# Performance work log

Measured on AMD Instinct MI355X. Metric: run time of the kernel, lower is better.

## Reference

```python
import jax, jax.numpy as jnp
import numpy as np

N, E = 50000, 800000
IN_F, HID, NCLS, NLAYERS = 64, 64, 2, 3
BN_EPS = 1e-5


def batch_norm(x, gamma, beta):
    # training-mode BatchNorm1d: biased batch statistics over the node/edge dim
    m = jnp.mean(x, axis=0)
    v = jnp.var(x, axis=0)
    return gamma * (x - m) * jax.lax.rsqrt(v + BN_EPS) + beta


def setup_inputs() -> dict:
    key = jax.random.key(0)
    ks = jax.random.split(key, 24)
    L, Lp1 = NLAYERS, NLAYERS + 1

    def lin(k, fan_in, shape):
        bound = 1.0 / np.sqrt(fan_in)
        return jax.random.uniform(k, shape, jnp.float32, -bound, bound)

    return {
        "h": jax.random.normal(ks[0], (N, IN_F), jnp.float32),
        "src": jax.random.randint(ks[1], (E,), 0, N, jnp.int32),
        "dst": jax.random.randint(ks[2], (E,), 0, N, jnp.int32),
        "emb_W": lin(ks[3], IN_F, (IN_F, HID)),
        "emb_b": lin(ks[4], IN_F, (HID,)),
        "mlp_W1": lin(ks[5], HID, (L, HID, HID)),
        "mlp_b1": lin(ks[6], HID, (L, HID)),
        "mlp_bn_g": jnp.ones((L, HID), jnp.float32),
        "mlp_bn_b": jnp.zeros((L, HID), jnp.float32),
        "mlp_W2": lin(ks[7], HID, (L, HID, HID)),
        "mlp_b2": lin(ks[8], HID, (L, HID)),
        "apply_bn_g": jnp.ones((L, HID), jnp.float32),
        "apply_bn_b": jnp.zeros((L, HID), jnp.float32),
        "out_bn_g": jnp.ones((L, HID), jnp.float32),
        "out_bn_b": jnp.zeros((L, HID), jnp.float32),
        "pred_W1": lin(ks[9], 2 * HID, (Lp1, 2 * HID, HID)),
        "pred_b1": lin(ks[10], 2 * HID, (Lp1, HID)),
        "pred_W2": lin(ks[11], HID, (Lp1, HID, NCLS)),
        "pred_b2": lin(ks[12], HID, (Lp1, NCLS)),
    }


def reference(h, src, dst, emb_W, emb_b, mlp_W1, mlp_b1, mlp_bn_g, mlp_bn_b,
              mlp_W2, mlp_b2, apply_bn_g, apply_bn_b, out_bn_g, out_bn_b,
              pred_W1, pred_b1, pred_W2, pred_b2):
    n_layers = mlp_W1.shape[0]
    n_nodes = h.shape[0]

    def edge_feat(hn):
        # concat src and dst node features per edge -> [E, 2*HID]
        return jnp.concatenate([hn[src], hn[dst]], axis=1)

    hn = h @ emb_W + emb_b  # embedding_h
    edge_reps = [edge_feat(hn)]

    for i in range(n_layers):
        # GINConv (sum aggregation, eps=0): (1+eps)*h_v + sum_{u->v} h_u
        agg = jax.ops.segment_sum(hn[src], dst, num_segments=n_nodes)
        z = hn + agg
        # MLP (depth 2): Linear -> BN -> ReLU -> Linear
        z = jax.nn.relu(batch_norm(z @ mlp_W1[i] + mlp_b1[i], mlp_bn_g[i], mlp_bn_b[i]))
        z = z @ mlp_W2[i] + mlp_b2[i]
        # ApplyNodeFunc: BN + ReLU
        z = jax.nn.relu(batch_norm(z, apply_bn_g[i], apply_bn_b[i]))
        # outer per-layer BN + ReLU
        hn = jax.nn.relu(batch_norm(z, out_bn_g[i], out_bn_b[i]))
        edge_reps.append(edge_feat(hn))

    # sum of per-layer edge predictions: Linear(2h->h) -> ReLU -> Linear(h->ncls)
    score = jnp.zeros((src.shape[0], pred_W2.shape[-1]), h.dtype)
    for i, e in enumerate(edge_reps):
        score = score + jax.nn.relu(e @ pred_W1[i] + pred_b1[i]) @ pred_W2[i] + pred_b2[i]
    return score
```

## Files before the change

kernel.cpp:

```cpp
#include <hip/hip_runtime.h>
#include <hip/hip_bf16.h>


#define BN_EPS 1e-5f

static __device__ __forceinline__ float bf2f_lo(unsigned u) {
  return __uint_as_float(u << 16);
}
static __device__ __forceinline__ float bf2f_hi(unsigned u) {
  return __uint_as_float(u & 0xffff0000u);
}

__global__ __launch_bounds__(256) void hist_kernel(const int* __restrict__ dst,
                                                   int* __restrict__ deg, int E) {
  int i = blockIdx.x * blockDim.x + threadIdx.x;
  int stride = gridDim.x * blockDim.x;
  for (; i < E; i += stride) atomicAdd(&deg[dst[i]], 1);
}

__global__ __launch_bounds__(256) void scan1_kernel(const int* __restrict__ deg,
                                                    int* __restrict__ rowstart,
                                                    int* __restrict__ partials, int N) {
  __shared__ int wsum[4];
  int tid = threadIdx.x;
  int lane = tid & 63, w = tid >> 6;
  int base = blockIdx.x * 1024 + tid * 4;
  int d0 = 0, d1 = 0, d2 = 0, d3 = 0;
  if (base + 3 < N) {
    int4 v = *reinterpret_cast<const int4*>(deg + base);
    d0 = v.x; d1 = v.y; d2 = v.z; d3 = v.w;
  } else {
    if (base + 0 < N) d0 = deg[base + 0];
    if (base + 1 < N) d1 = deg[base + 1];
    if (base + 2 < N) d2 = deg[base + 2];
  }
  int t0 = d0, t1 = t0 + d1, t2 = t1 + d2, t3 = t2 + d3;
  int tot = t3;
  int inc = tot;
#pragma unroll
  for (int off = 1; off < 64; off <<= 1) {
    int v = __shfl_up(inc, off);
    if (lane >= off) inc += v;
  }
  if (lane == 63) wsum[w] = inc;
  __syncthreads();
  int woff = 0;
  for (int k = 0; k < w; ++k) woff += wsum[k];
  int excl = woff + inc - tot;
  if (base + 0 < N) rowstart[base + 0] = excl;
  if (base + 1 < N) rowstart[base + 1] = excl + t0;
  if (base + 2 < N) rowstart[base + 2] = excl + t1;
  if (base + 3 < N) rowstart[base + 3] = excl + t2;
  if (tid == 255) partials[blockIdx.x] = excl + t3;
}

__global__ __launch_bounds__(256) void scan3_kernel(const int* __restrict__ partials,
                                                    int* __restrict__ rowstart,
                                                    int* __restrict__ cursor,
                                                    int N, int NB, int E) {
  __shared__ int s_off;
  int tid = threadIdx.x;
  if (tid < 64) {
    int v = (tid < NB) ? partials[tid] : 0;
    int inc = v;
#pragma unroll
    for (int off = 1; off < 64; off <<= 1) {
      int t = __shfl_up(inc, off);
      if (tid >= off) inc += t;
    }
    if (tid == (int)blockIdx.x) s_off = inc - v;
  }
  __syncthreads();
  int off = s_off;
  int base = blockIdx.x * 1024 + tid * 4;
#pragma unroll
  for (int k = 0; k < 4; ++k) {
    int i = base + k;
    if (i < N) {
      int r = rowstart[i] + off;
      rowstart[i] = r;
      cursor[i] = r;
    }
  }
  if (blockIdx.x == 0 && tid == 0) rowstart[N] = E;
}

__global__ __launch_bounds__(256) void fill_kernel(const int* __restrict__ src,
                                                   const int* __restrict__ dst,
                                                   int* __restrict__ cursor,
                                                   int2* __restrict__ epack, int E) {
  int i = blockIdx.x * blockDim.x + threadIdx.x;
  int stride = gridDim.x * blockDim.x;
  for (; i < E; i += stride) {
    int p = atomicAdd(&cursor[dst[i]], 1);
    epack[p] = make_int2(src[i], i);
  }
}

__global__ __launch_bounds__(256) void gemm64_kernel(
    const float* __restrict__ in, const float* __restrict__ W,
    const float* __restrict__ bias, const float* __restrict__ stats_in,
    const float* __restrict__ g_in, const float* __restrict__ b_in,
    float* __restrict__ out, float* __restrict__ stats_out,
    ushort* __restrict__ out_g, int N) {
  __shared__ float sW[64][64];
  __shared__ float sx[32][64];
  __shared__ float red[2][4][64];
  int tid = threadIdx.x;
  int lane = tid & 63, w = tid >> 6;
  int n0 = blockIdx.x * 32;
#pragma unroll
  for (int r = 0; r < 16; ++r) {
    int idx = r * 256 + tid;
    sW[idx >> 6][idx & 63] = W[idx];
  }
  float sc = 1.f, sh = 0.f;
  if (stats_in) {
    float invN = 1.0f / (float)N;
    float m = stats_in[lane] * invN;
    float var = stats_in[64 + lane] * invN - m * m;
    sc = g_in[lane] * rsqrtf(var + BN_EPS);
    sh = b_in[lane] - m * sc;
  }
#pragma unroll
  for (int r = 0; r < 8; ++r) {
    int idx = r * 256 + tid;
    int n = n0 + (idx >> 6);
    float x = (n < N) ? in[(size_t)n * 64 + lane] : 0.f;
    if (stats_in) x = fmaxf(x * sc + sh, 0.f);
    sx[idx >> 6][lane] = x;
  }
  __syncthreads();
  float acc[8];
  float bz = bias ? bias[lane] : 0.f;
#pragma unroll
  for (int j = 0; j < 8; ++j) acc[j] = bz;
  for (int k = 0; k < 64; ++k) {
    float wv = sW[k][lane];
#pragma unroll
    for (int j = 0; j < 8; ++j) acc[j] = fmaf(sx[w * 8 + j][k], wv, acc[j]);
  }
  float ps = 0.f, pq = 0.f;
#pragma unroll
  for (int j = 0; j < 8; ++j) {
    int n = n0 + w * 8 + j;
    if (n < N) {
      out[(size_t)n * 64 + lane] = acc[j];
      if (out_g) {
        __hip_bfloat16 b = __float2bfloat16(acc[j]);
        out_g[(size_t)n * 128 + lane] = *reinterpret_cast<ushort*>(&b);
      }
      ps += acc[j];
      pq += acc[j] * acc[j];
    }
  }
  if (stats_out) {
    red[0][w][lane] = ps;
    red[1][w][lane] = pq;
    __syncthreads();
    if (w == 0) {
      float s = red[0][0][lane] + red[0][1][lane] + red[0][2][lane] + red[0][3][lane];
      float q = red[1][0][lane] + red[1][1][lane] + red[1][2][lane] + red[1][3][lane];
      atomicAdd(&stats_out[lane], s);
      atomicAdd(&stats_out[64 + lane], q);
    }
  }
}

__global__ __launch_bounds__(256) void proj_kernel(
    const float* __restrict__ c, const float* __restrict__ W1,
    const float* __restrict__ b1, const float* __restrict__ stats_in,
    const float* __restrict__ g_in, const float* __restrict__ b_in,
    ushort* __restrict__ G, ushort* __restrict__ P2, int N) {
  __shared__ float sWa[64][64];
  __shared__ float sWb[64][64];
  __shared__ float sx[32][64];
  int tid = threadIdx.x, lane = tid & 63, w = tid >> 6;
  int n0 = blockIdx.x * 32;
#pragma unroll
  for (int r = 0; r < 16; ++r) {
    int idx = r * 256 + tid;
    sWa[idx >> 6][idx & 63] = W1[idx];
    sWb[idx >> 6][idx & 63] = W1[4096 + idx];
  }
  float sc = 1.f, sh = 0.f;
  if (stats_in) {
    float invN = 1.0f / (float)N;
    float m = stats_in[lane] * invN;
    float var = stats_in[64 + lane] * invN - m * m;
    sc = g_in[lane] * rsqrtf(var + BN_EPS);
    sh = b_in[lane] - m * sc;
  }
#pragma unroll
  for (int r = 0; r < 8; ++r) {
    int idx = r * 256 + tid;
    int n = n0 + (idx >> 6);
    float x = (n < N) ? c[(size_t)n * 64 + lane] : 0.f;
    if (stats_in) x = fmaxf(x * sc + sh, 0.f);
    sx[idx >> 6][lane] = x;
  }
  __syncthreads();
  float a1[8], a2[8];
  float bz = b1[lane];
#pragma unroll
  for (int j = 0; j < 8; ++j) { a1[j] = bz; a2[j] = 0.f; }
  for (int k = 0; k < 64; ++k) {
    float wa = sWa[k][lane];
    float wb = sWb[k][lane];
#pragma unroll
    for (int j = 0; j < 8; ++j) {
      float x = sx[w * 8 + j][k];
      a1[j] = fmaf(x, wa, a1[j]);
      a2[j] = fmaf(x, wb, a2[j]);
    }
  }
#pragma unroll
  for (int j = 0; j < 8; ++j) {
    int n = n0 + w * 8 + j;
    if (n < N) {
      __hip_bfloat16 b1v = __float2bfloat16(a1[j]);
      __hip_bfloat16 b2v = __float2bfloat16(a2[j]);
      G[(size_t)n * 128 + lane] = *reinterpret_cast<ushort*>(&b1v);
      P2[(size_t)n * 64 + lane] = *reinterpret_cast<ushort*>(&b2v);
    }
  }
}

__global__ __launch_bounds__(256) void bnrelu_kernel(
    const float* __restrict__ in, const float* __restrict__ stats_in,
    const float* __restrict__ g_in, const float* __restrict__ b_in,
    float* __restrict__ out, float* __restrict__ stats_out,
    ushort* __restrict__ out_g, int N) {
  __shared__ float red[2][4][64];
  int tid = threadIdx.x;
  int lane = tid & 63, w = tid >> 6;
  float invN = 1.0f / (float)N;
  float m = stats_in[lane] * invN;
  float var = stats_in[64 + lane] * invN - m * m;
  float sc = g_in[lane] * rsqrtf(var + BN_EPS);
  float sh = b_in[lane] - m * sc;
  float ps = 0.f, pq = 0.f;
  int rows_per_grid = gridDim.x * (blockDim.x >> 6);
  for (int n = blockIdx.x * (blockDim.x >> 6) + w; n < N; n += rows_per_grid) {
    float x = fmaxf(in[(size_t)n * 64 + lane] * sc + sh, 0.f);
    out[(size_t)n * 64 + lane] = x;
    __hip_bfloat16 b = __float2bfloat16(x);
    out_g[(size_t)n * 128 + lane] = *reinterpret_cast<ushort*>(&b);
    ps += x;
    pq += x * x;
  }
  if (stats_out) {
    red[0][w][lane] = ps;
    red[1][w][lane] = pq;
    __syncthreads();
    if (w == 0) {
      float s = red[0][0][lane] + red[0][1][lane] + red[0][2][lane] + red[0][3][lane];
      float q = red[1][0][lane] + red[1][1][lane] + red[1][2][lane] + red[1][3][lane];
      atomicAdd(&stats_out[lane], s);
      atomicAdd(&stats_out[64 + lane], q);
    }
  }
}

template <int TR>
__global__ __launch_bounds__(256) void score_agg_kernel(
    const ushort* __restrict__ G, const ushort* __restrict__ P2,
    const float* __restrict__ c, const int* __restrict__ rowstart,
    const int2* __restrict__ epack, const float* __restrict__ W2,
    const float* __restrict__ b2, const float* __restrict__ stats_tr,
    const float* __restrict__ g_tr, const float* __restrict__ b_tr,
    float2* __restrict__ sc, float* __restrict__ zb, int N, int first) {
  int lane = threadIdx.x & 63;
  int v = blockIdx.x * 4 + (threadIdx.x >> 6);
  if (v >= N) return;
  int grp = lane >> 4;
  int g16 = lane & 15;
  int sub = g16 & 7;
  float w[16];
  {
    const float4* wp = reinterpret_cast<const float4*>(W2 + sub * 16);
#pragma unroll
    for (int k = 0; k < 4; ++k) {
      float4 t = wp[k];
      w[4 * k + 0] = t.x; w[4 * k + 1] = t.y; w[4 * k + 2] = t.z; w[4 * k + 3] = t.w;
    }
  }
  float bb0 = b2[0], bb1 = b2[1];
  uint4 pb = *reinterpret_cast<const uint4*>(P2 + (size_t)v * 64 + sub * 8);
  unsigned bv[4] = {pb.x, pb.y, pb.z, pb.w};
  float scv[8], shv[8];
  if (TR) {
    float invN = 1.0f / (float)N;
#pragma unroll
    for (int k = 0; k < 8; ++k) {
      int f = sub * 8 + k;
      float m = stats_tr[f] * invN;
      float var = stats_tr[64 + f] * invN - m * m;
      scv[k] = g_tr[f] * rsqrtf(var + BN_EPS);
      shv[k] = b_tr[f] - m * scv[k];
    }
  }
  float acc[8];
#pragma unroll
  for (int k = 0; k < 8; ++k) acc[k] = 0.f;

  int p0 = rowstart[v], p1 = rowstart[v + 1];
  for (int p = p0 + grp; p < p1; p += 4) {
    int s = epack[p].x;
    uint4 row = *reinterpret_cast<const uint4*>(G + (size_t)s * 128 + g16 * 8);
    unsigned rv[4] = {row.x, row.y, row.z, row.w};
    float q0 = 0.f, q1 = 0.f;
    if (g16 < 8) {
#pragma unroll
      for (int k = 0; k < 4; ++k) {
        float v0 = fmaxf(bf2f_lo(rv[k]) + bf2f_lo(bv[k]), 0.f);
        float v1 = fmaxf(bf2f_hi(rv[k]) + bf2f_hi(bv[k]), 0.f);
        q0 = fmaf(v0, w[4 * k + 0], fmaf(v1, w[4 * k + 2], q0));
        q1 = fmaf(v0, w[4 * k + 1], fmaf(v1, w[4 * k + 3], q1));
      }
    } else {
#pragma unroll
      for (int k = 0; k < 4; ++k) {
        float x0 = bf2f_lo(rv[k]);
        float x1 = bf2f_hi(rv[k]);
        if (TR) {
          x0 = fmaxf(x0 * scv[2 * k] + shv[2 * k], 0.f);
          x1 = fmaxf(x1 * scv[2 * k + 1] + shv[2 * k + 1], 0.f);
        }
        acc[2 * k] += x0;
        acc[2 * k + 1] += x1;
      }
    }
#pragma unroll
    for (int mm = 1; mm < 8; mm <<= 1) {
      q0 += __shfl_xor(q0, mm);
      q1 += __shfl_xor(q1, mm);
    }
    if (g16 == 0) {
      float o0 = q0 + bb0, o1 = q1 + bb1;
      if (!first) {
        float2 prev = sc[p];
        o0 += prev.x;
        o1 += prev.y;
      }
      sc[p] = make_float2(o0, o1);
    }
  }
#pragma unroll
  for (int k = 0; k < 8; ++k) {
    acc[k] += __shfl_xor(acc[k], 16);
    acc[k] += __shfl_xor(acc[k], 32);
  }
  if (grp == 0 && g16 >= 8) {
    const float* cv = c + (size_t)v * 64 + sub * 8;
    float4 c0 = *reinterpret_cast<const float4*>(cv);
    float4 c1 = *reinterpret_cast<const float4*>(cv + 4);
    float cf[8] = {c0.x, c0.y, c0.z, c0.w, c1.x, c1.y, c1.z, c1.w};
    float ov[8];
#pragma unroll
    for (int k = 0; k < 8; ++k) {
      float x = cf[k];
      if (TR) x = fmaxf(x * scv[k] + shv[k], 0.f);
      ov[k] = acc[k] + x;
    }
    float* zp = zb + (size_t)v * 64 + sub * 8;
    *reinterpret_cast<float4*>(zp) = make_float4(ov[0], ov[1], ov[2], ov[3]);
    *reinterpret_cast<float4*>(zp + 4) = make_float4(ov[4], ov[5], ov[6], ov[7]);
  }
}

__global__ __launch_bounds__(256) void edge_score_csr_kernel(
    const ushort* __restrict__ G, const ushort* __restrict__ P2,
    const int* __restrict__ rowstart, const int2* __restrict__ epack,
    const float* __restrict__ W2, const float* __restrict__ b2,
    float2* __restrict__ sc, int N, int first) {
  int lane = threadIdx.x & 63;
  int v = blockIdx.x * 4 + (threadIdx.x >> 6);
  if (v >= N) return;
  int sub = lane & 7;
  int grp = lane >> 3;
  float w[16];
  const float4* wp = reinterpret_cast<const float4*>(W2 + sub * 16);
#pragma unroll
  for (int k = 0; k < 4; ++k) {
    float4 t = wp[k];
    w[4 * k + 0] = t.x; w[4 * k + 1] = t.y; w[4 * k + 2] = t.z; w[4 * k + 3] = t.w;
  }
  float bb0 = b2[0], bb1 = b2[1];
  uint4 pb = *reinterpret_cast<const uint4*>(P2 + (size_t)v * 64 + sub * 8);
  unsigned bv[4] = {pb.x, pb.y, pb.z, pb.w};
  int p0 = rowstart[v], p1 = rowstart[v + 1];
  for (int p = p0 + grp; p < p1; p += 8) {
    int s = epack[p].x;
    uint4 pa = *reinterpret_cast<const uint4*>(G + (size_t)s * 128 + sub * 8);
    unsigned av[4] = {pa.x, pa.y, pa.z, pa.w};
    float q0 = 0.f, q1 = 0.f;
#pragma unroll
    for (int k = 0; k < 4; ++k) {
      float v0 = fmaxf(bf2f_lo(av[k]) + bf2f_lo(bv[k]), 0.f);
      float v1 = fmaxf(bf2f_hi(av[k]) + bf2f_hi(bv[k]), 0.f);
      q0 = fmaf(v0, w[4 * k + 0], fmaf(v1, w[4 * k + 2], q0));
      q1 = fmaf(v0, w[4 * k + 1], fmaf(v1, w[4 * k + 3], q1));
    }
#pragma unroll
    for (int mm = 1; mm < 8; mm <<= 1) {
      q0 += __shfl_xor(q0, mm);
      q1 += __shfl_xor(q1, mm);
    }
    if (sub == 0) {
      float o0 = q0 + bb0, o1 = q1 + bb1;
      if (!first) {
        float2 prev = sc[p];
        o0 += prev.x;
        o1 += prev.y;
      }
      sc[p] = make_float2(o0, o1);
    }
  }
}

__global__ __launch_bounds__(256) void scatter_kernel(const float2* __restrict__ sc,
                                                      const int2* __restrict__ epack,
                                                      float2* __restrict__ out, int E) {
  int i = blockIdx.x * blockDim.x + threadIdx.x;
  int stride = gridDim.x * blockDim.x;
  for (; i < E; i += stride) out[epack[i].y] = sc[i];
}

extern "C" void kernel_launch(void* const* d_in, const int* in_sizes, int n_in,
                              void* d_out, int out_size, void* d_ws, size_t ws_size,
                              hipStream_t stream) {
  const float* h          = (const float*)d_in[0];
  const int*   src        = (const int*)d_in[1];
  const int*   dst        = (const int*)d_in[2];
  const float* emb_W      = (const float*)d_in[3];
  const float* emb_b      = (const float*)d_in[4];
  const float* mlp_W1     = (const float*)d_in[5];
  const float* mlp_b1     = (const float*)d_in[6];
  const float* mlp_bn_g   = (const float*)d_in[7];
  const float* mlp_bn_b   = (const float*)d_in[8];
  const float* mlp_W2     = (const float*)d_in[9];
  const float* mlp_b2     = (const float*)d_in[10];
  const float* apply_bn_g = (const float*)d_in[11];
  const float* apply_bn_b = (const float*)d_in[12];
  const float* out_bn_g   = (const float*)d_in[13];
  const float* out_bn_b   = (const float*)d_in[14];
  const float* pred_W1    = (const float*)d_in[15];
  const float* pred_b1    = (const float*)d_in[16];
  const float* pred_W2    = (const float*)d_in[17];
  const float* pred_b2    = (const float*)d_in[18];

  const int N = in_sizes[0] / 64;
  const int E = in_sizes[1];
  const size_t NF = (size_t)N * 64;
  const int NB1 = (N + 1023) / 1024;

  float* ws = (float*)d_ws;
  float* c   = ws;
  float* z1  = c + NF;
  float* zb  = z1 + NF;
  ushort* G  = (ushort*)(zb + NF);
  ushort* P2 = G + (size_t)N * 128;
  int2*   epack = (int2*)(P2 + NF);
  float2* scbuf = (float2*)(epack + E);
  int* rowstart = (int*)(scbuf + E);
  int* cursor   = rowstart + (N + 64);
  int* partials = cursor + (N + 64);
  int* deg      = partials + 64;
  float* stats  = (float*)(deg + (N + 64));

  size_t need = (size_t)((char*)(stats + 9 * 128) - (char*)d_ws);
  if (need > ws_size) return;

  hipMemsetAsync(deg, 0, ((size_t)(N + 64) + 9 * 128) * sizeof(int), stream);

  const int gemmBlocks = (N + 31) / 32;
  const int nodeBlocks = (N + 3) / 4;

  gemm64_kernel<<<gemmBlocks, 256, 0, stream>>>(h, emb_W, emb_b, nullptr, nullptr,
                                                nullptr, c, nullptr, G + 64, N);
  hist_kernel<<<1024, 256, 0, stream>>>(dst, deg, E);
  scan1_kernel<<<NB1, 256, 0, stream>>>(deg, rowstart, partials, N);
  scan3_kernel<<<NB1, 256, 0, stream>>>(partials, rowstart, cursor, N, NB1, E);
  fill_kernel<<<1024, 256, 0, stream>>>(src, dst, cursor, epack, E);

  proj_kernel<<<gemmBlocks, 256, 0, stream>>>(c, pred_W1, pred_b1, nullptr, nullptr,
                                              nullptr, G, P2, N);
  score_agg_kernel<0><<<nodeBlocks, 256, 0, stream>>>(
      G, P2, c, rowstart, epack, pred_W2, pred_b2, nullptr, nullptr, nullptr,
      scbuf, zb, N, 1);

  for (int i = 0; i < 3; ++i) {
    float* st1 = stats + (size_t)(3 * i + 0) * 128;
    float* st2 = stats + (size_t)(3 * i + 1) * 128;
    float* st3 = stats + (size_t)(3 * i + 2) * 128;

    gemm64_kernel<<<gemmBlocks, 256, 0, stream>>>(zb, mlp_W1 + (size_t)i * 4096,
                                                  mlp_b1 + i * 64, nullptr, nullptr,
                                                  nullptr, z1, st1, nullptr, N);
    gemm64_kernel<<<gemmBlocks, 256, 0, stream>>>(z1, mlp_W2 + (size_t)i * 4096,
                                                  mlp_b2 + i * 64, st1,
                                                  mlp_bn_g + i * 64, mlp_bn_b + i * 64,
                                                  zb, st2, nullptr, N);
    bnrelu_kernel<<<784, 256, 0, stream>>>(zb, st2, apply_bn_g + i * 64,
                                           apply_bn_b + i * 64, c, st3, G + 64, N);
    proj_kernel<<<gemmBlocks, 256, 0, stream>>>(c, pred_W1 + (size_t)(i + 1) * 8192,
                                                pred_b1 + (i + 1) * 64, st3,
                                                out_bn_g + i * 64, out_bn_b + i * 64,
                                                G, P2, N);
    if (i < 2) {
      score_agg_kernel<1><<<nodeBlocks, 256, 0, stream>>>(
          G, P2, c, rowstart, epack, pred_W2 + (i + 1) * 128,
          pred_b2 + (i + 1) * 2, st3, out_bn_g + i * 64, out_bn_b + i * 64,
          scbuf, zb, N, 0);
    } else {
      edge_score_csr_kernel<<<nodeBlocks, 256, 0, stream>>>(
          G, P2, rowstart, epack, pred_W2 + (i + 1) * 128,
          pred_b2 + (i + 1) * 2, scbuf, N, 0);
    }
  }

  scatter_kernel<<<2048, 256, 0, stream>>>(scbuf, epack, (float2*)d_out, E);
}
```

Baseline: 926.2 us.

## Register-tile node GEMMs 4x4 and fuse final edge score with output scatter

The 64-wide node GEMM and projection kernels now use a transposed, padded shared-memory input tile. Each block covers 64 rows, and each thread computes a 4x4 output tile using float4 shared loads and vectorized stores. This cuts LDS traffic per FMA and the number of blocks launched. Separately, the last-layer edge score kernel adds the accumulated scores and writes straight to the output in original edge order, which removes the separate scatter kernel and its pass over scbuf. The cost is higher register pressure from the 16 or 32 accumulators and uncoalesced writes from the final kernel.

```diff
diff --git a/kernel.cpp b/kernel.cpp
--- a/kernel.cpp
+++ b/kernel.cpp
@@ -9,6 +9,10 @@
 }
 static __device__ __forceinline__ float bf2f_hi(unsigned u) {
   return __uint_as_float(u & 0xffff0000u);
+}
+static __device__ __forceinline__ ushort f2bf(float x) {
+  __hip_bfloat16 b = __float2bfloat16(x);
+  return *reinterpret_cast<ushort*>(&b);
 }
 
 __global__ __launch_bounds__(256) void hist_kernel(const int* __restrict__ dst,
@@ -104,11 +108,11 @@
     float* __restrict__ out, float* __restrict__ stats_out,
     ushort* __restrict__ out_g, int N) {
   __shared__ float sW[64][64];
-  __shared__ float sx[32][64];
-  __shared__ float red[2][4][64];
+  __shared__ float sxT[64][68];
+  __shared__ float red[2][16][64];
   int tid = threadIdx.x;
   int lane = tid & 63, w = tid >> 6;
-  int n0 = blockIdx.x * 32;
+  int n0 = blockIdx.x * 64;
 #pragma unroll
   for (int r = 0; r < 16; ++r) {
     int idx = r * 256 + tid;
@@ -123,46 +127,76 @@
     sh = b_in[lane] - m * sc;
   }
 #pragma unroll
-  for (int r = 0; r < 8; ++r) {
+  for (int r = 0; r < 16; ++r) {
     int idx = r * 256 + tid;
-    int n = n0 + (idx >> 6);
+    int row = idx >> 6;
+    int n = n0 + row;
     float x = (n < N) ? in[(size_t)n * 64 + lane] : 0.f;
     if (stats_in) x = fmaxf(x * sc + sh, 0.f);
-    sx[idx >> 6][lane] = x;
+    sxT[lane][row] = x;
   }
   __syncthreads();
-  float acc[8];
-  float bz = bias ? bias[lane] : 0.f;
-#pragma unroll
-  for (int j = 0; j < 8; ++j) acc[j] = bz;
+  int tc = lane & 15, tr = lane >> 4;
+  int rowbase = w * 16 + tr * 4;
+  int colbase = tc * 4;
+  float acc[16];
+  if (bias) {
+    float4 bz = *reinterpret_cast<const float4*>(bias + colbase);
+#pragma unroll
+    for (int rr = 0; rr < 4; ++rr) {
+      acc[rr * 4 + 0] = bz.x; acc[rr * 4 + 1] = bz.y;
+      acc[rr * 4 + 2] = bz.z; acc[rr * 4 + 3] = bz.w;
+    }
+  } else {
+#pragma unroll
+    for (int i = 0; i < 16; ++i) acc[i] = 0.f;
+  }
+#pragma unroll 8
   for (int k = 0; k < 64; ++k) {
-    float wv = sW[k][lane];
-#pragma unroll
-    for (int j = 0; j < 8; ++j) acc[j] = fmaf(sx[w * 8 + j][k], wv, acc[j]);
-  }
-  float ps = 0.f, pq = 0.f;
-#pragma unroll
-  for (int j = 0; j < 8; ++j) {
-    int n = n0 + w * 8 + j;
+    float4 xv = *reinterpret_cast<const float4*>(&sxT[k][rowbase]);
+    float4 wv = *reinterpret_cast<const float4*>(&sW[k][colbase]);
+    acc[0]  = fmaf(xv.x, wv.x, acc[0]);  acc[1]  = fmaf(xv.x, wv.y, acc[1]);
+    acc[2]  = fmaf(xv.x, wv.z, acc[2]);  acc[3]  = fmaf(xv.x, wv.w, acc[3]);
+    acc[4]  = fmaf(xv.y, wv.x, acc[4]);  acc[5]  = fmaf(xv.y, wv.y, acc[5]);
+    acc[6]  = fmaf(xv.y, wv.z, acc[6]);  acc[7]  = fmaf(xv.y, wv.w, acc[7]);
+    acc[8]  = fmaf(xv.z, wv.x, acc[8]);  acc[9]  = fmaf(xv.z, wv.y, acc[9]);
+    acc[10] = fmaf(xv.z, wv.z, acc[10]); acc[11] = fmaf(xv.z, wv.w, acc[11]);
+    acc[12] = fmaf(xv.w, wv.x, acc[12]); acc[13] = fmaf(xv.w, wv.y, acc[13]);
+    acc[14] = fmaf(xv.w, wv.z, acc[14]); acc[15] = fmaf(xv.w, wv.w, acc[15]);
+  }
+  float ps[4] = {0.f, 0.f, 0.f, 0.f}, pq[4] = {0.f, 0.f, 0.f, 0.f};
+#pragma unroll
+  for (int rr = 0; rr < 4; ++rr) {
+    int n = n0 + rowbase + rr;
     if (n < N) {
-      out[(size_t)n * 64 + lane] = acc[j];
+      float4 o = make_float4(acc[rr * 4 + 0], acc[rr * 4 + 1],
+                             acc[rr * 4 + 2], acc[rr * 4 + 3]);
+      *reinterpret_cast<float4*>(out + (size_t)n * 64 + colbase) = o;
       if (out_g) {
-        __hip_bfloat16 b = __float2bfloat16(acc[j]);
-        out_g[(size_t)n * 128 + lane] = *reinterpret_cast<ushort*>(&b);
+        uint2 pk;
+        pk.x = (unsigned)f2bf(o.x) | ((unsigned)f2bf(o.y) << 16);
+        pk.y = (unsigned)f2bf(o.z) | ((unsigned)f2bf(o.w) << 16);
+        *reinterpret_cast<uint2*>(out_g + (size_t)n * 128 + colbase) = pk;
       }
-      ps += acc[j];
-      pq += acc[j] * acc[j];
+      ps[0] += o.x; ps[1] += o.y; ps[2] += o.z; ps[3] += o.w;
+      pq[0] += o.x * o.x; pq[1] += o.y * o.y;
+      pq[2] += o.z * o.z; pq[3] += o.w * o.w;
     }
   }
   if (stats_out) {
-    red[0][w][lane] = ps;
-    red[1][w][lane] = pq;
+    int rg = w * 4 + tr;
+#pragma unroll
+    for (int cc = 0; cc < 4; ++cc) {
+      red[0][rg][colbase + cc] = ps[cc];
+      red[1][rg][colbase + cc] = pq[cc];
+    }
     __syncthreads();
-    if (w == 0) {
-      float s = red[0][0][lane] + red[0][1][lane] + red[0][2][lane] + red[0][3][lane];
-      float q = red[1][0][lane] + red[1][1][lane] + red[1][2][lane] + red[1][3][lane];
-      atomicAdd(&stats_out[lane], s);
-      atomicAdd(&stats_out[64 + lane], q);
+    if (tid < 128) {
+      int s = tid >> 6, col = tid & 63;
+      float acc2 = 0.f;
+#pragma unroll
+      for (int g = 0; g < 16; ++g) acc2 += red[s][g][col];
+      atomicAdd(&stats_out[s * 64 + col], acc2);
     }
   }
 }
@@ -174,9 +208,9 @@
     ushort* __restrict__ G, ushort* __restrict__ P2, int N) {
   __shared__ float sWa[64][64];
   __shared__ float sWb[64][64];
-  __shared__ float sx[32][64];
+  __shared__ float sxT[64][68];
   int tid = threadIdx.x, lane = tid & 63, w = tid >> 6;
-  int n0 = blockIdx.x * 32;
+  int n0 = blockIdx.x * 64;
 #pragma unroll
   for (int r = 0; r < 16; ++r) {
     int idx = r * 256 + tid;
@@ -192,36 +226,62 @@
     sh = b_in[lane] - m * sc;
   }
 #pragma unroll
-  for (int r = 0; r < 8; ++r) {
+  for (int r = 0; r < 16; ++r) {
     int idx = r * 256 + tid;
-    int n = n0 + (idx >> 6);
+    int row = idx >> 6;
+    int n = n0 + row;
     float x = (n < N) ? c[(size_t)n * 64 + lane] : 0.f;
     if (stats_in) x = fmaxf(x * sc + sh, 0.f);
-    sx[idx >> 6][lane] = x;
+    sxT[lane][row] = x;
   }
   __syncthreads();
-  float a1[8], a2[8];
-  float bz = b1[lane];
-#pragma unroll
-  for (int j = 0; j < 8; ++j) { a1[j] = bz; a2[j] = 0.f; }
+  int tc = lane & 15, tr = lane >> 4;
+  int rowbase = w * 16 + tr * 4;
+  int colbase = tc * 4;
+  float a1[16], a2[16];
+  {
+    float4 bz = *reinterpret_cast<const float4*>(b1 + colbase);
+#pragma unroll
+    for (int rr = 0; rr < 4; ++rr) {
+      a1[rr * 4 + 0] = bz.x; a1[rr * 4 + 1] = bz.y;
+      a1[rr * 4 + 2] = bz.z; a1[rr * 4 + 3] = bz.w;
+    }
+#pragma unroll
+    for (int i = 0; i < 16; ++i) a2[i] = 0.f;
+  }
+#pragma unroll 4
   for (int k = 0; k < 64; ++k) {
-    float wa = sWa[k][lane];
-    float wb = sWb[k][lane];
-#pragma unroll
-    for (int j = 0; j < 8; ++j) {
-      float x = sx[w * 8 + j][k];
-      a1[j] = fmaf(x, wa, a1[j]);
-      a2[j] = fmaf(x, wb, a2[j]);
-    }
-  }
-#pragma unroll
-  for (int j = 0; j < 8; ++j) {
-    int n = n0 + w * 8 + j;
+    float4 xv = *reinterpret_cast<const float4*>(&sxT[k][rowbase]);
+    float4 wa = *reinterpret_cast<const float4*>(&sWa[k][colbase]);
+    float4 wb = *reinterpret_cast<const float4*>(&sWb[k][colbase]);
+    a1[0]  = fmaf(xv.x, wa.x, a1[0]);  a1[1]  = fmaf(xv.x, wa.y, a1[1]);
+    a1[2]  = fmaf(xv.x, wa.z, a1[2]);  a1[3]  = fmaf(xv.x, wa.w, a1[3]);
+    a1[4]  = fmaf(xv.y, wa.x, a1[4]);  a1[5]  = fmaf(xv.y, wa.y, a1[5]);
+    a1[6]  = fmaf(xv.y, wa.z, a1[6]);  a1[7]  = fmaf(xv.y, wa.w, a1[7]);
+    a1[8]  = fmaf(xv.z, wa.x, a1[8]);  a1[9]  = fmaf(xv.z, wa.y, a1[9]);
+    a1[10] = fmaf(xv.z, wa.z, a1[10]); a1[11] = fmaf(xv.z, wa.w, a1[11]);
+    a1[12] = fmaf(xv.w, wa.x, a1[12]); a1[13] = fmaf(xv.w, wa.y, a1[13]);
+    a1[14] = fmaf(xv.w, wa.z, a1[14]); a1[15] = fmaf(xv.w, wa.w, a1[15]);
+    a2[0]  = fmaf(xv.x, wb.x, a2[0]);  a2[1]  = fmaf(xv.x, wb.y, a2[1]);
+    a2[2]  = fmaf(xv.x, wb.z, a2[2]);  a2[3]  = fmaf(xv.x, wb.w, a2[3]);
+    a2[4]  = fmaf(xv.y, wb.x, a2[4]);  a2[5]  = fmaf(xv.y, wb.y, a2[5]);
+    a2[6]  = fmaf(xv.y, wb.z, a2[6]);  a2[7]  = fmaf(xv.y, wb.w, a2[7]);
+    a2[8]  = fmaf(xv.z, wb.x, a2[8]);  a2[9]  = fmaf(xv.z, wb.y, a2[9]);
+    a2[10] = fmaf(xv.z, wb.z, a2[10]); a2[11] = fmaf(xv.z, wb.w, a2[11]);
+    a2[12] = fmaf(xv.w, wb.x, a2[12]); a2[13] = fmaf(xv.w, wb.y, a2[13]);
+    a2[14] = fmaf(xv.w, wb.z, a2[14]); a2[15] = fmaf(xv.w, wb.w, a2[15]);
+  }
+#pragma unroll
+  for (int rr = 0; rr < 4; ++rr) {
+    int n = n0 + rowbase + rr;
     if (n < N) {
-      __hip_bfloat16 b1v = __float2bfloat16(a1[j]);
-      __hip_bfloat16 b2v = __float2bfloat16(a2[j]);
-      G[(size_t)n * 128 + lane] = *reinterpret_cast<ushort*>(&b1v);
-      P2[(size_t)n * 64 + lane] = *reinterpret_cast<ushort*>(&b2v);
+      uint2 p1k, p2k;
+      p1k.x = (unsigned)f2bf(a1[rr * 4 + 0]) | ((unsigned)f2bf(a1[rr * 4 + 1]) << 16);
+      p1k.y = (unsigned)f2bf(a1[rr * 4 + 2]) | ((unsigned)f2bf(a1[rr * 4 + 3]) << 16);
+      p2k.x = (unsigned)f2bf(a2[rr * 4 + 0]) | ((unsigned)f2bf(a2[rr * 4 + 1]) << 16);
+      p2k.y = (unsigned)f2bf(a2[rr * 4 + 2]) | ((unsigned)f2bf(a2[rr * 4 + 3]) << 16);
+      *reinterpret_cast<uint2*>(G + (size_t)n * 128 + colbase) = p1k;
+      *reinterpret_cast<uint2*>(P2 + (size_t)n * 64 + colbase) = p2k;
     }
   }
 }
@@ -244,8 +304,7 @@
   for (int n = blockIdx.x * (blockDim.x >> 6) + w; n < N; n += rows_per_grid) {
     float x = fmaxf(in[(size_t)n * 64 + lane] * sc + sh, 0.f);
     out[(size_t)n * 64 + lane] = x;
-    __hip_bfloat16 b = __float2bfloat16(x);
-    out_g[(size_t)n * 128 + lane] = *reinterpret_cast<ushort*>(&b);
+    out_g[(size_t)n * 128 + lane] = f2bf(x);
     ps += x;
     pq += x * x;
   }
@@ -369,11 +428,11 @@
   }
 }
 
-__global__ __launch_bounds__(256) void edge_score_csr_kernel(
+__global__ __launch_bounds__(256) void edge_score_final_kernel(
     const ushort* __restrict__ G, const ushort* __restrict__ P2,
     const int* __restrict__ rowstart, const int2* __restrict__ epack,
     const float* __restrict__ W2, const float* __restrict__ b2,
-    float2* __restrict__ sc, int N, int first) {
+    const float2* __restrict__ sc, float2* __restrict__ out, int N) {
   int lane = threadIdx.x & 63;
   int v = blockIdx.x * 4 + (threadIdx.x >> 6);
   if (v >= N) return;
@@ -391,7 +450,8 @@
   unsigned bv[4] = {pb.x, pb.y, pb.z, pb.w};
   int p0 = rowstart[v], p1 = rowstart[v + 1];
   for (int p = p0 + grp; p < p1; p += 8) {
-    int s = epack[p].x;
+    int2 ep = epack[p];
+    int s = ep.x;
     uint4 pa = *reinterpret_cast<const uint4*>(G + (size_t)s * 128 + sub * 8);
     unsigned av[4] = {pa.x, pa.y, pa.z, pa.w};
     float q0 = 0.f, q1 = 0.f;
@@ -408,23 +468,10 @@
       q1 += __shfl_xor(q1, mm);
     }
     if (sub == 0) {
-      float o0 = q0 + bb0, o1 = q1 + bb1;
-      if (!first) {
-        float2 prev = sc[p];
-        o0 += prev.x;
-        o1 += prev.y;
-      }
-      sc[p] = make_float2(o0, o1);
-    }
-  }
-}
-
-__global__ __launch_bounds__(256) void scatter_kernel(const float2* __restrict__ sc,
-                                                      const int2* __restrict__ epack,
-                                                      float2* __restrict__ out, int E) {
-  int i = blockIdx.x * blockDim.x + threadIdx.x;
-  int stride = gridDim.x * blockDim.x;
-  for (; i < E; i += stride) out[epack[i].y] = sc[i];
+      float2 prev = sc[p];
+      out[ep.y] = make_float2(q0 + bb0 + prev.x, q1 + bb1 + prev.y);
+    }
+  }
 }
 
 extern "C" void kernel_launch(void* const* d_in, const int* in_sizes, int n_in,
@@ -474,7 +521,7 @@
 
   hipMemsetAsync(deg, 0, ((size_t)(N + 64) + 9 * 128) * sizeof(int), stream);
 
-  const int gemmBlocks = (N + 31) / 32;
+  const int gemmBlocks = (N + 63) / 64;
   const int nodeBlocks = (N + 3) / 4;
 
   gemm64_kernel<<<gemmBlocks, 256, 0, stream>>>(h, emb_W, emb_b, nullptr, nullptr,
@@ -514,11 +561,9 @@
           pred_b2 + (i + 1) * 2, st3, out_bn_g + i * 64, out_bn_b + i * 64,
           scbuf, zb, N, 0);
     } else {
-      edge_score_csr_kernel<<<nodeBlocks, 256, 0, stream>>>(
+      edge_score_final_kernel<<<nodeBlocks, 256, 0, stream>>>(
           G, P2, rowstart, epack, pred_W2 + (i + 1) * 128,
-          pred_b2 + (i + 1) * 2, scbuf, N, 0);
-    }
-  }
-
-  scatter_kernel<<<2048, 256, 0, stream>>>(scbuf, epack, (float2*)d_out, E);
-}
+          pred_b2 + (i + 1) * 2, scbuf, (float2*)d_out, N);
+    }
+  }
+}
```

New measurement: 843.2 us. -9.0%, faster.
